# Optimization experiments

Hardware: AMD Instinct MI355X
Metric: run time of the kernel (lower is better)

The kernel has to match this reference:

```python
import jax, jax.numpy as jnp
import numpy as np

D_MODEL = 256; N_HEADS = 8; N_LEVELS = 4; N_POINTS = 4
D_HEAD = D_MODEL // N_HEADS


def setup_inputs() -> dict:
    key = jax.random.key(0)
    ks = jax.random.split(key, 8)
    N, Lq = 4, 4096
    shapes = np.array([4096, 2048, 1024, 512], dtype=np.int32)  # temporal lengths per level
    Len_in = int(shapes.sum())  # 7680
    start = np.concatenate([[0], np.cumsum(shapes)[:-1]]).astype(np.int32)
    HLP = N_HEADS * N_LEVELS * N_POINTS
    return {
        "query": jax.random.normal(ks[0], (N, Lq, D_MODEL), jnp.float32),
        "reference_points": jax.random.uniform(ks[1], (N, Lq, N_LEVELS, 1), jnp.float32),
        "input_flatten": jax.random.normal(ks[2], (N, Len_in, D_MODEL), jnp.float32),
        "input_spatial_shapes": jnp.asarray(shapes),
        "input_level_start_index": jnp.asarray(start),
        "W_off": jax.random.normal(ks[3], (D_MODEL, HLP), jnp.float32) * 0.01,
        "b_off": jax.random.normal(ks[4], (HLP,), jnp.float32) * 2.0,
        "W_aw": jax.random.normal(ks[5], (D_MODEL, HLP), jnp.float32) * 0.02,
        "b_aw": jnp.zeros((HLP,), jnp.float32),
        "W_v": jax.random.normal(ks[6], (D_MODEL, D_MODEL), jnp.float32) / np.sqrt(D_MODEL).astype(np.float32),
        "b_v": jnp.zeros((D_MODEL,), jnp.float32),
        "W_out": jax.random.normal(ks[7], (D_MODEL, D_MODEL), jnp.float32) / np.sqrt(D_MODEL).astype(np.float32),
        "b_out": jnp.zeros((D_MODEL,), jnp.float32),
    }


def reference(query, reference_points, input_flatten, input_spatial_shapes,
              input_level_start_index, W_off, b_off, W_aw, b_aw, W_v, b_v,
              W_out, b_out):
    N, Lq, C = query.shape
    M, L, P, Dh = N_HEADS, N_LEVELS, N_POINTS, D_HEAD
    S = input_flatten.shape[1]

    value = (input_flatten @ W_v + b_v).reshape(N, S, M, Dh)
    off = (query @ W_off + b_off).reshape(N, Lq, M, L, P)
    aw = jax.nn.softmax((query @ W_aw + b_aw).reshape(N, Lq, M, L * P), axis=-1)
    aw = aw.reshape(N, Lq, M, L, P)

    # reference_points last dim == 1 branch: loc = ref + off / T_l, in [0,1]
    T = input_spatial_shapes.astype(jnp.float32)[None, None, None, :, None]  # [1,1,1,L,1]
    loc = reference_points[:, :, None, :, None, 0] + off / T  # [N,Lq,M,L,P]

    # grid_sample(align_corners=False, padding_mode='border') along W with H=1, y=0.5:
    # pixel coord x = loc*T - 0.5, clamped to [0, T-1], then linear interp.
    x = jnp.clip(loc * T - 0.5, 0.0, T - 1.0)
    x0 = jnp.floor(x)
    w1 = x - x0                                   # frac weight for right neighbor
    i0 = x0.astype(jnp.int32)
    i1 = jnp.minimum(i0 + 1, input_spatial_shapes[None, None, None, :, None] - 1)
    base = input_level_start_index[None, None, None, :, None]
    g0 = i0 + base                                # global flattened indices [N,Lq,M,L,P]
    g1 = i1 + base

    v = value.transpose(0, 2, 1, 3)               # [N,M,S,Dh]

    def gather(idx):
        idxt = idx.transpose(0, 2, 1, 3, 4).reshape(N, M, Lq * L * P, 1)
        return jnp.take_along_axis(v, idxt, axis=2).reshape(N, M, Lq, L, P, Dh)

    s0 = gather(g0)
    s1 = gather(g1)
    w1t = w1.transpose(0, 2, 1, 3, 4)[..., None]   # [N,M,Lq,L,P,1]
    samp = s0 * (1.0 - w1t) + s1 * w1t             # [N,M,Lq,L,P,Dh]

    awt = aw.transpose(0, 2, 1, 3, 4)[..., None]
    out = (samp * awt).sum(axis=(3, 4))            # [N,M,Lq,Dh]
    out = out.transpose(0, 2, 1, 3).reshape(N, Lq, M * Dh)
    return out @ W_out + b_out
```

## Files before the change

kernel.cpp:

```cpp
#include <hip/hip_runtime.h>
#include <hip/hip_bf16.h>
#include <cstddef>
#include <cstdint>

#define D_MODEL   256
#define N_HEADS   8
#define N_LEVELS  4
#define N_POINTS  4
#define D_HEAD    32
#define HLP       128
#define NBATCH    4
#define LQ        4096
#define S_LEN     7680
#define QB        8

typedef __attribute__((ext_vector_type(8))) short  short8;
typedef __attribute__((ext_vector_type(4))) float  f32x4;
typedef __attribute__((ext_vector_type(8))) unsigned short ushort8;

__device__ __forceinline__ unsigned short f2bf(float x) {
    __hip_bfloat16 h = __float2bfloat16(x);
    return *reinterpret_cast<unsigned short*>(&h);
}
__device__ __forceinline__ float bf2f(unsigned short u) {
    unsigned int v = ((unsigned int)u) << 16;
    return *reinterpret_cast<float*>(&v);
}

__device__ __forceinline__ void gload_lds16(const void* g, void* l) {
    __builtin_amdgcn_global_load_lds(
        (const __attribute__((address_space(1))) void*)g,
        (__attribute__((address_space(3))) void*)l,
        16, 0, 0);
}

__global__ __launch_bounds__(256) void prep_kernel(
    const float* __restrict__ W_v,  const float* __restrict__ W_off,
    const float* __restrict__ W_aw, const float* __restrict__ W_out,
    const float* __restrict__ b_off, const float* __restrict__ b_aw,
    unsigned short* __restrict__ Wv_t, unsigned short* __restrict__ Wcat_t,
    unsigned short* __restrict__ Wout_t, float* __restrict__ bcat)
{
    __shared__ float t[64][65];
    const int z   = blockIdx.z;
    const int k0  = blockIdx.y * 64;
    const int n0  = blockIdx.x * 64;
    const int tid = threadIdx.x;

    const float* src; int srcN; int cs; unsigned short* dst;
    if (z == 0)      { src = W_v;   srcN = 256; cs = n0;       dst = Wv_t;  }
    else if (z == 2) { src = W_out; srcN = 256; cs = n0;       dst = Wout_t;}
    else if (n0 < 128){ src = W_off; srcN = 128; cs = n0;      dst = Wcat_t;}
    else             { src = W_aw;  srcN = 128; cs = n0 - 128; dst = Wcat_t;}

    #pragma unroll
    for (int i = 0; i < 16; ++i) {
        int idx = tid + i * 256;
        int kk = idx >> 6, nn = idx & 63;
        t[kk][nn] = src[(size_t)(k0 + kk) * srcN + cs + nn];
    }
    __syncthreads();
    #pragma unroll
    for (int i = 0; i < 16; ++i) {
        int idx = tid + i * 256;
        int nn = idx >> 6, kk = idx & 63;
        dst[(size_t)(n0 + nn) * 256 + k0 + kk] = f2bf(t[kk][nn]);
    }
    if (z == 1 && blockIdx.x == 0 && blockIdx.y == 0) {
        bcat[tid] = (tid < 128) ? b_off[tid] : b_aw[tid - 128];
    }
}

__global__ __launch_bounds__(256) void gemm_vp_kernel(
    const float* __restrict__ inflat, const float* __restrict__ query,
    const unsigned short* __restrict__ Wv_t, const unsigned short* __restrict__ Wcat_t,
    const float* __restrict__ b_v, const float* __restrict__ bcat,
    unsigned short* __restrict__ value3, float* __restrict__ P)
{
    __shared__ alignas(16) unsigned short Abuf[2][4][64][8];
    __shared__ alignas(16) unsigned short Bbuf[2][8][64][8];

    const int job = blockIdx.x;
    const bool is_val = (job < 960);
    const int jj   = is_val ? job : (job - 960);
    const int row0 = (jj >> 1) * 64;
    const int col0 = (jj & 1) * 128;
    const float* A = is_val ? inflat : query;
    const unsigned short* Bt = is_val ? Wv_t : Wcat_t;
    const float* bias = is_val ? b_v : bcat;

    const int tid  = threadIdx.x;
    const int lane = tid & 63;
    const int w    = tid >> 6;
    const int lr   = lane & 15;
    const int lk   = (lane >> 4) * 8;

    const int ar = tid >> 2;
    const int ak = (tid & 3) * 8;
    const int afrag = ar >> 4;
    const int alane = ((ak >> 3) << 4) | (ar & 15);
    const float* Arow = A + (size_t)(row0 + ar) * 256 + ak;
    const unsigned short* Bcol = Bt + (size_t)(col0 + lr) * 256 + lk;

    f32x4 acc[8] = {};

    float4 pa0 = *(const float4*)(Arow);
    float4 pa1 = *(const float4*)(Arow + 4);
    #pragma unroll
    for (int c = 0; c < 2; ++c) {
        const int in = w * 2 + c;
        gload_lds16(Bcol + (size_t)in * 16 * 256, &Bbuf[0][in][0][0]);
    }

    for (int kt = 0; kt < 8; ++kt) {
        const int cur = kt & 1;
        short8 pk;
        pk[0] = (short)f2bf(pa0.x); pk[1] = (short)f2bf(pa0.y);
        pk[2] = (short)f2bf(pa0.z); pk[3] = (short)f2bf(pa0.w);
        pk[4] = (short)f2bf(pa1.x); pk[5] = (short)f2bf(pa1.y);
        pk[6] = (short)f2bf(pa1.z); pk[7] = (short)f2bf(pa1.w);
        *(short8*)&Abuf[cur][afrag][alane][0] = pk;
        __syncthreads();

        if (kt < 7) {
            const int k1 = (kt + 1) * 32;
            pa0 = *(const float4*)(Arow + k1);
            pa1 = *(const float4*)(Arow + k1 + 4);
            #pragma unroll
            for (int c = 0; c < 2; ++c) {
                const int in = w * 2 + c;
                gload_lds16(Bcol + (size_t)in * 16 * 256 + k1, &Bbuf[1 - cur][in][0][0]);
            }
        }

        const short8 af = *(const short8*)&Abuf[cur][w][lane][0];
        #pragma unroll
        for (int j = 0; j < 8; ++j) {
            const short8 bf = *(const short8*)&Bbuf[cur][j][lane][0];
            acc[j] = __builtin_amdgcn_mfma_f32_16x16x32_bf16(af, bf, acc[j], 0, 0, 0);
        }
    }

    const int prow = (lane >> 4) * 4;
    const int pcol = lane & 15;
    const int rbase = row0 + w * 16 + prow;
    if (is_val) {
        const int n  = row0 / S_LEN;
        const int s0 = row0 - n * S_LEN + w * 16 + prow;
        #pragma unroll
        for (int j = 0; j < 8; ++j) {
            const int col = col0 + j * 16 + pcol;
            const float bs = bias[col];
            const int m = col >> 5, d = col & 31;
            unsigned short* dst = value3 + ((size_t)(n * 8 + m) * S_LEN + s0) * 32 + d;
            #pragma unroll
            for (int r = 0; r < 4; ++r)
                dst[(size_t)r * 32] = f2bf(acc[j][r] + bs);
        }
    } else {
        #pragma unroll
        for (int j = 0; j < 8; ++j) {
            const int col = col0 + j * 16 + pcol;
            const float bs = bias[col];
            #pragma unroll
            for (int r = 0; r < 4; ++r)
                P[(size_t)(rbase + r) * 256 + col] = acc[j][r] + bs;
        }
    }
}

__global__ __launch_bounds__(256) void sample_kernel(
    const float* __restrict__ P, const float* __restrict__ refp,
    const int* __restrict__ shapes, const int* __restrict__ lstart,
    const unsigned short* __restrict__ value3,
    unsigned short* __restrict__ tout)
{
    __shared__ int   sG0[QB][130];
    __shared__ float sW [QB][130];
    __shared__ float sA [QB][130];
    __shared__ int   glim[4];

    const int b    = blockIdx.x;
    const int xcd  = b & 7;
    const int n    = xcd >> 1;
    const int half = xcd & 1;
    const int slot = b >> 3;
    const int q0   = (slot * 2 + half) * QB;
    const int nq0  = n * LQ + q0;
    const int tid  = threadIdx.x;

    if (tid < 4) glim[tid] = lstart[tid] + shapes[tid] - 1;

    #pragma unroll
    for (int it = 0; it < 4; ++it) {
        const int idx = tid + it * 256;
        const int q   = idx >> 7;
        const int j   = idx & 127;
        const int l   = (j >> 2) & 3;
        const int nq  = nq0 + q;
        const float off   = __builtin_nontemporal_load(P + (size_t)nq * 256 + j);
        const float logit = __builtin_nontemporal_load(P + (size_t)nq * 256 + 128 + j);
        const float ref   = __builtin_nontemporal_load(refp + (size_t)nq * N_LEVELS + l);
        const int   sh    = shapes[l];
        const float Tf    = (float)sh;
        float x = ref * Tf + off - 0.5f;
        x = fminf(fmaxf(x, 0.0f), Tf - 1.0f);
        const float x0 = floorf(x);
        sG0[q][j] = (int)x0 + lstart[l];
        sW [q][j] = x - x0;
        sA [q][j] = logit;
    }
    __syncthreads();

    const int q  = tid >> 5;
    const int r  = tid & 31;
    const int m  = r >> 2;
    const int ql = r & 3;
    const unsigned short* vb =
        value3 + (size_t)(n * 8 + m) * S_LEN * 32 + ql * 8;

    float e[16];
    float mx = -1e30f;
    #pragma unroll
    for (int i = 0; i < 16; ++i) { e[i] = sA[q][m * 16 + i]; mx = fmaxf(mx, e[i]); }
    float s = 0.f;
    #pragma unroll
    for (int i = 0; i < 16; ++i) { e[i] = __expf(e[i] - mx); s += e[i]; }
    const float rs = 1.0f / s;

    float acc[8] = {};
    #pragma unroll
    for (int i = 0; i < 16; ++i) {
        const int j = m * 16 + i;
        const float a  = e[i] * rs;
        const float ww = sW[q][j];
        const int g0 = sG0[q][j];
        const int g1 = min(g0 + 1, glim[i >> 2]);
        const ushort8 u0 = *(const ushort8*)(vb + (size_t)g0 * 32);
        const ushort8 u1 = *(const ushort8*)(vb + (size_t)g1 * 32);
        #pragma unroll
        for (int d = 0; d < 8; ++d) {
            const float v0 = bf2f(u0[d]);
            const float v1 = bf2f(u1[d]);
            acc[d] += a * (v0 + ww * (v1 - v0));
        }
    }
    ushort8 o;
    #pragma unroll
    for (int d = 0; d < 8; ++d) o[d] = f2bf(acc[d]);
    __builtin_nontemporal_store(o,
        (ushort8*)(tout + (size_t)(nq0 + q) * 256 + m * 32 + ql * 8));
}

__global__ __launch_bounds__(256) void gemm_out_kernel(
    const unsigned short* __restrict__ A,
    const unsigned short* __restrict__ Bt,
    const float* __restrict__ bias,
    float* __restrict__ Cout)
{
    __shared__ alignas(16) unsigned short Abuf[2][4][64][8];
    __shared__ alignas(16) unsigned short Bbuf[2][8][64][8];

    const int jj   = blockIdx.x;
    const int row0 = (jj >> 1) * 64;
    const int col0 = (jj & 1) * 128;

    const int tid  = threadIdx.x;
    const int lane = tid & 63;
    const int w    = tid >> 6;
    const int lr   = lane & 15;
    const int lk   = (lane >> 4) * 8;

    const unsigned short* Arow = A + (size_t)(row0 + w * 16 + lr) * 256 + lk;
    const unsigned short* Bcol = Bt + (size_t)(col0 + lr) * 256 + lk;

    f32x4 acc[8] = {};

    gload_lds16(Arow, &Abuf[0][w][0][0]);
    #pragma unroll
    for (int c = 0; c < 2; ++c) {
        const int in = w * 2 + c;
        gload_lds16(Bcol + (size_t)in * 16 * 256, &Bbuf[0][in][0][0]);
    }

    for (int kt = 0; kt < 8; ++kt) {
        const int cur = kt & 1;
        __syncthreads();

        if (kt < 7) {
            const int k1 = (kt + 1) * 32;
            gload_lds16(Arow + k1, &Abuf[1 - cur][w][0][0]);
            #pragma unroll
            for (int c = 0; c < 2; ++c) {
                const int in = w * 2 + c;
                gload_lds16(Bcol + (size_t)in * 16 * 256 + k1, &Bbuf[1 - cur][in][0][0]);
            }
        }

        const short8 af = *(const short8*)&Abuf[cur][w][lane][0];
        #pragma unroll
        for (int j = 0; j < 8; ++j) {
            const short8 bf = *(const short8*)&Bbuf[cur][j][lane][0];
            acc[j] = __builtin_amdgcn_mfma_f32_16x16x32_bf16(af, bf, acc[j], 0, 0, 0);
        }
    }

    const int prow = (lane >> 4) * 4;
    const int pcol = lane & 15;
    const int rbase = row0 + w * 16 + prow;
    #pragma unroll
    for (int j = 0; j < 8; ++j) {
        const int col = col0 + j * 16 + pcol;
        const float bs = bias[col];
        #pragma unroll
        for (int r = 0; r < 4; ++r)
            Cout[(size_t)(rbase + r) * 256 + col] = acc[j][r] + bs;
    }
}

extern "C" void kernel_launch(void* const* d_in, const int* in_sizes, int n_in,
                              void* d_out, int out_size, void* d_ws, size_t ws_size,
                              hipStream_t stream)
{
    const float* query  = (const float*)d_in[0];
    const float* refp   = (const float*)d_in[1];
    const float* inflat = (const float*)d_in[2];
    const int*   shapes = (const int*)d_in[3];
    const int*   lstart = (const int*)d_in[4];
    const float* W_off  = (const float*)d_in[5];
    const float* b_off  = (const float*)d_in[6];
    const float* W_aw   = (const float*)d_in[7];
    const float* b_aw   = (const float*)d_in[8];
    const float* W_v    = (const float*)d_in[9];
    const float* b_v    = (const float*)d_in[10];
    const float* W_out  = (const float*)d_in[11];
    const float* b_out  = (const float*)d_in[12];

    const int M_val = NBATCH * S_LEN;
    const int M_q   = NBATCH * LQ;

    char* p = (char*)d_ws;
    unsigned short* value3 = (unsigned short*)p; p += (size_t)M_val * D_MODEL * 2;
    float*          P      = (float*)p;          p += (size_t)M_q * 256 * 4;
    unsigned short* tbuf   = (unsigned short*)p; p += (size_t)M_q * D_MODEL * 2;
    unsigned short* Wv_t   = (unsigned short*)p; p += 256 * 256 * 2;
    unsigned short* Wcat_t = (unsigned short*)p; p += 256 * 256 * 2;
    unsigned short* Wout_t = (unsigned short*)p; p += 256 * 256 * 2;
    float*          bcat   = (float*)p;          p += 256 * 4;

    prep_kernel<<<dim3(4, 4, 3), 256, 0, stream>>>(
        W_v, W_off, W_aw, W_out, b_off, b_aw, Wv_t, Wcat_t, Wout_t, bcat);
    gemm_vp_kernel<<<1472, 256, 0, stream>>>(
        inflat, query, Wv_t, Wcat_t, b_v, bcat, value3, P);
    sample_kernel<<<2048, 256, 0, stream>>>(
        P, refp, shapes, lstart, value3, tbuf);
    gemm_out_kernel<<<512, 256, 0, stream>>>(
        tbuf, Wout_t, b_out, (float*)d_out);
}
```

Measured before the change: 160.9 us.

## Assign one head per sampling block over 64 queries for value locality

The sampling kernel now gives each block a single head and 64 consecutive queries, instead of all 8 heads for 8 queries. Blocks are spread so that the XCD parity selects the head. Gathers from one block then stay inside one head's value slice, which should improve L2 locality. The prologue loads offsets and logits as float4 and writes them to LDS as vectors. The risk is narrower per-row P reads (64 bytes per query per block) and a grid mapping that must still match the launch size.

After: 163.6 us. No clear change (+1.7%).

```diff
diff --git a/kernel.cpp b/kernel.cpp
--- a/kernel.cpp
+++ b/kernel.cpp
@@ -12,10 +12,10 @@
 #define NBATCH    4
 #define LQ        4096
 #define S_LEN     7680
-#define QB        8
 
 typedef __attribute__((ext_vector_type(8))) short  short8;
 typedef __attribute__((ext_vector_type(4))) float  f32x4;
+typedef __attribute__((ext_vector_type(4))) int    i32x4;
 typedef __attribute__((ext_vector_type(8))) unsigned short ushort8;
 
 __device__ __forceinline__ unsigned short f2bf(float x) {
@@ -175,54 +175,71 @@
     const unsigned short* __restrict__ value3,
     unsigned short* __restrict__ tout)
 {
-    __shared__ int   sG0[QB][130];
-    __shared__ float sW [QB][130];
-    __shared__ float sA [QB][130];
+    __shared__ int   sG0[64][20];
+    __shared__ float sW [64][20];
+    __shared__ float sA [64][20];
     __shared__ int   glim[4];
 
     const int b    = blockIdx.x;
     const int xcd  = b & 7;
     const int n    = xcd >> 1;
-    const int half = xcd & 1;
-    const int slot = b >> 3;
-    const int q0   = (slot * 2 + half) * QB;
+    const int mpar = xcd & 1;
+    const int jb   = b >> 3;
+    const int m    = ((jb & 3) << 1) | mpar;
+    const int q0   = (jb >> 2) * 64;
     const int nq0  = n * LQ + q0;
     const int tid  = threadIdx.x;
 
     if (tid < 4) glim[tid] = lstart[tid] + shapes[tid] - 1;
 
-    #pragma unroll
-    for (int it = 0; it < 4; ++it) {
-        const int idx = tid + it * 256;
-        const int q   = idx >> 7;
-        const int j   = idx & 127;
-        const int l   = (j >> 2) & 3;
-        const int nq  = nq0 + q;
-        const float off   = __builtin_nontemporal_load(P + (size_t)nq * 256 + j);
-        const float logit = __builtin_nontemporal_load(P + (size_t)nq * 256 + 128 + j);
-        const float ref   = __builtin_nontemporal_load(refp + (size_t)nq * N_LEVELS + l);
+    {
+        const int q  = tid >> 2;
+        const int l  = tid & 3;
+        const int i0 = l * 4;
+        const int nq = nq0 + q;
+        const f32x4 off   = __builtin_nontemporal_load(
+            (const f32x4*)(P + (size_t)nq * 256 + m * 16 + i0));
+        const f32x4 logit = __builtin_nontemporal_load(
+            (const f32x4*)(P + (size_t)nq * 256 + 128 + m * 16 + i0));
+        const float ref   = refp[(size_t)nq * N_LEVELS + l];
         const int   sh    = shapes[l];
+        const int   ls    = lstart[l];
         const float Tf    = (float)sh;
-        float x = ref * Tf + off - 0.5f;
-        x = fminf(fmaxf(x, 0.0f), Tf - 1.0f);
-        const float x0 = floorf(x);
-        sG0[q][j] = (int)x0 + lstart[l];
-        sW [q][j] = x - x0;
-        sA [q][j] = logit;
+        i32x4 g4; f32x4 w4;
+        #pragma unroll
+        for (int k = 0; k < 4; ++k) {
+            float x = ref * Tf + off[k] - 0.5f;
+            x = fminf(fmaxf(x, 0.0f), Tf - 1.0f);
+            const float x0 = floorf(x);
+            g4[k] = (int)x0 + ls;
+            w4[k] = x - x0;
+        }
+        *(i32x4*)&sG0[q][i0] = g4;
+        *(f32x4*)&sW [q][i0] = w4;
+        *(f32x4*)&sA [q][i0] = logit;
     }
     __syncthreads();
 
-    const int q  = tid >> 5;
-    const int r  = tid & 31;
-    const int m  = r >> 2;
-    const int ql = r & 3;
+    const int q  = tid >> 2;
+    const int ql = tid & 3;
+    const int nq = nq0 + q;
     const unsigned short* vb =
         value3 + (size_t)(n * 8 + m) * S_LEN * 32 + ql * 8;
 
     float e[16];
+    {
+        const f32x4 a0 = *(const f32x4*)&sA[q][0];
+        const f32x4 a1 = *(const f32x4*)&sA[q][4];
+        const f32x4 a2 = *(const f32x4*)&sA[q][8];
+        const f32x4 a3 = *(const f32x4*)&sA[q][12];
+        #pragma unroll
+        for (int k = 0; k < 4; ++k) {
+            e[k] = a0[k]; e[4+k] = a1[k]; e[8+k] = a2[k]; e[12+k] = a3[k];
+        }
+    }
     float mx = -1e30f;
     #pragma unroll
-    for (int i = 0; i < 16; ++i) { e[i] = sA[q][m * 16 + i]; mx = fmaxf(mx, e[i]); }
+    for (int i = 0; i < 16; ++i) mx = fmaxf(mx, e[i]);
     float s = 0.f;
     #pragma unroll
     for (int i = 0; i < 16; ++i) { e[i] = __expf(e[i] - mx); s += e[i]; }
@@ -231,10 +248,9 @@
     float acc[8] = {};
     #pragma unroll
     for (int i = 0; i < 16; ++i) {
-        const int j = m * 16 + i;
         const float a  = e[i] * rs;
-        const float ww = sW[q][j];
-        const int g0 = sG0[q][j];
+        const float ww = sW[q][i];
+        const int g0 = sG0[q][i];
         const int g1 = min(g0 + 1, glim[i >> 2]);
         const ushort8 u0 = *(const ushort8*)(vb + (size_t)g0 * 32);
         const ushort8 u1 = *(const ushort8*)(vb + (size_t)g1 * 32);
@@ -249,7 +265,7 @@
     #pragma unroll
     for (int d = 0; d < 8; ++d) o[d] = f2bf(acc[d]);
     __builtin_nontemporal_store(o,
-        (ushort8*)(tout + (size_t)(nq0 + q) * 256 + m * 32 + ql * 8));
+        (ushort8*)(tout + (size_t)nq * 256 + m * 32 + ql * 8));
 }
 
 __global__ __launch_bounds__(256) void gemm_out_kernel(
```

## Fuse deformable sampling with output projection GEMM via LDS staging

Applied to the files above, without the earlier changes.

Merges the sampling kernel and the output-projection GEMM into one kernel. Each block now handles 16 queries, stages the sampled bf16 result in LDS and runs MFMA against W_out, read straight from global memory. This removes the intermediate tbuf round-trip through HBM and one kernel launch. The offset and logit loads are also vectorised to float4. In exchange, every block rereads the full W_out matrix (from cache), and the grid is halved to 1024 blocks, which lowers parallelism.

Measured after the change: 162.3 us. About the same (+0.9%).

```diff
diff --git a/kernel.cpp b/kernel.cpp
--- a/kernel.cpp
+++ b/kernel.cpp
@@ -12,10 +12,10 @@
 #define NBATCH    4
 #define LQ        4096
 #define S_LEN     7680
-#define QB        8
 
 typedef __attribute__((ext_vector_type(8))) short  short8;
 typedef __attribute__((ext_vector_type(4))) float  f32x4;
+typedef __attribute__((ext_vector_type(4))) int    i32x4;
 typedef __attribute__((ext_vector_type(8))) unsigned short ushort8;
 
 __device__ __forceinline__ unsigned short f2bf(float x) {
@@ -169,15 +169,18 @@
     }
 }
 
-__global__ __launch_bounds__(256) void sample_kernel(
+__global__ __launch_bounds__(256) void sample_out_kernel(
     const float* __restrict__ P, const float* __restrict__ refp,
     const int* __restrict__ shapes, const int* __restrict__ lstart,
     const unsigned short* __restrict__ value3,
-    unsigned short* __restrict__ tout)
+    const unsigned short* __restrict__ Wout_t,
+    const float* __restrict__ b_out,
+    float* __restrict__ Cout)
 {
-    __shared__ int   sG0[QB][130];
-    __shared__ float sW [QB][130];
-    __shared__ float sA [QB][130];
+    __shared__ int   sG0[16][132];
+    __shared__ float sW [16][132];
+    __shared__ float sA [16][132];
+    __shared__ alignas(16) unsigned short t_lds[16][264];
     __shared__ int   glim[4];
 
     const int b    = blockIdx.x;
@@ -185,136 +188,130 @@
     const int n    = xcd >> 1;
     const int half = xcd & 1;
     const int slot = b >> 3;
-    const int q0   = (slot * 2 + half) * QB;
+    const int q0   = (slot * 2 + half) * 16;
     const int nq0  = n * LQ + q0;
     const int tid  = threadIdx.x;
 
     if (tid < 4) glim[tid] = lstart[tid] + shapes[tid] - 1;
 
     #pragma unroll
-    for (int it = 0; it < 4; ++it) {
+    for (int it = 0; it < 2; ++it) {
         const int idx = tid + it * 256;
-        const int q   = idx >> 7;
-        const int j   = idx & 127;
-        const int l   = (j >> 2) & 3;
+        const int q   = idx >> 5;
+        const int sub = idx & 31;
+        const int m   = sub >> 2;
+        const int l   = sub & 3;
+        const int j0  = m * 16 + l * 4;
         const int nq  = nq0 + q;
-        const float off   = __builtin_nontemporal_load(P + (size_t)nq * 256 + j);
-        const float logit = __builtin_nontemporal_load(P + (size_t)nq * 256 + 128 + j);
-        const float ref   = __builtin_nontemporal_load(refp + (size_t)nq * N_LEVELS + l);
+        const f32x4 off   = __builtin_nontemporal_load(
+            (const f32x4*)(P + (size_t)nq * 256 + j0));
+        const f32x4 logit = __builtin_nontemporal_load(
+            (const f32x4*)(P + (size_t)nq * 256 + 128 + j0));
+        const float ref   = refp[(size_t)nq * N_LEVELS + l];
         const int   sh    = shapes[l];
+        const int   ls    = lstart[l];
         const float Tf    = (float)sh;
-        float x = ref * Tf + off - 0.5f;
-        x = fminf(fmaxf(x, 0.0f), Tf - 1.0f);
-        const float x0 = floorf(x);
-        sG0[q][j] = (int)x0 + lstart[l];
-        sW [q][j] = x - x0;
-        sA [q][j] = logit;
+        i32x4 g4; f32x4 w4;
+        #pragma unroll
+        for (int k = 0; k < 4; ++k) {
+            float x = ref * Tf + off[k] - 0.5f;
+            x = fminf(fmaxf(x, 0.0f), Tf - 1.0f);
+            const float x0 = floorf(x);
+            g4[k] = (int)x0 + ls;
+            w4[k] = x - x0;
+        }
+        *(i32x4*)&sG0[q][j0] = g4;
+        *(f32x4*)&sW [q][j0] = w4;
+        *(f32x4*)&sA [q][j0] = logit;
     }
     __syncthreads();
 
-    const int q  = tid >> 5;
-    const int r  = tid & 31;
-    const int m  = r >> 2;
-    const int ql = r & 3;
-    const unsigned short* vb =
-        value3 + (size_t)(n * 8 + m) * S_LEN * 32 + ql * 8;
-
-    float e[16];
-    float mx = -1e30f;
-    #pragma unroll
-    for (int i = 0; i < 16; ++i) { e[i] = sA[q][m * 16 + i]; mx = fmaxf(mx, e[i]); }
-    float s = 0.f;
-    #pragma unroll
-    for (int i = 0; i < 16; ++i) { e[i] = __expf(e[i] - mx); s += e[i]; }
-    const float rs = 1.0f / s;
-
-    float acc[8] = {};
-    #pragma unroll
-    for (int i = 0; i < 16; ++i) {
-        const int j = m * 16 + i;
-        const float a  = e[i] * rs;
-        const float ww = sW[q][j];
-        const int g0 = sG0[q][j];
-        const int g1 = min(g0 + 1, glim[i >> 2]);
-        const ushort8 u0 = *(const ushort8*)(vb + (size_t)g0 * 32);
-        const ushort8 u1 = *(const ushort8*)(vb + (size_t)g1 * 32);
-        #pragma unroll
-        for (int d = 0; d < 8; ++d) {
-            const float v0 = bf2f(u0[d]);
-            const float v1 = bf2f(u1[d]);
-            acc[d] += a * (v0 + ww * (v1 - v0));
-        }
-    }
-    ushort8 o;
-    #pragma unroll
-    for (int d = 0; d < 8; ++d) o[d] = f2bf(acc[d]);
-    __builtin_nontemporal_store(o,
-        (ushort8*)(tout + (size_t)(nq0 + q) * 256 + m * 32 + ql * 8));
-}
-
-__global__ __launch_bounds__(256) void gemm_out_kernel(
-    const unsigned short* __restrict__ A,
-    const unsigned short* __restrict__ Bt,
-    const float* __restrict__ bias,
-    float* __restrict__ Cout)
-{
-    __shared__ alignas(16) unsigned short Abuf[2][4][64][8];
-    __shared__ alignas(16) unsigned short Bbuf[2][8][64][8];
-
-    const int jj   = blockIdx.x;
-    const int row0 = (jj >> 1) * 64;
-    const int col0 = (jj & 1) * 128;
-
-    const int tid  = threadIdx.x;
+    #pragma unroll
+    for (int it = 0; it < 2; ++it) {
+        const int idx = tid + it * 256;
+        const int q   = idx >> 5;
+        const int sub = idx & 31;
+        const int m   = sub >> 2;
+        const int ql  = sub & 3;
+        const unsigned short* vb =
+            value3 + (size_t)(n * 8 + m) * S_LEN * 32 + ql * 8;
+
+        float e[16];
+        {
+            const f32x4 a0 = *(const f32x4*)&sA[q][m * 16 + 0];
+            const f32x4 a1 = *(const f32x4*)&sA[q][m * 16 + 4];
+            const f32x4 a2 = *(const f32x4*)&sA[q][m * 16 + 8];
+            const f32x4 a3 = *(const f32x4*)&sA[q][m * 16 + 12];
+            #pragma unroll
+            for (int k = 0; k < 4; ++k) {
+                e[k] = a0[k]; e[4+k] = a1[k]; e[8+k] = a2[k]; e[12+k] = a3[k];
+            }
+        }
+        float mx = -1e30f;
+        #pragma unroll
+        for (int i = 0; i < 16; ++i) mx = fmaxf(mx, e[i]);
+        float s = 0.f;
+        #pragma unroll
+        for (int i = 0; i < 16; ++i) { e[i] = __expf(e[i] - mx); s += e[i]; }
+        const float rs = 1.0f / s;
+
+        float acc[8] = {};
+        #pragma unroll
+        for (int i = 0; i < 16; ++i) {
+            const int j = m * 16 + i;
+            const float a  = e[i] * rs;
+            const float ww = sW[q][j];
+            const int g0 = sG0[q][j];
+            const int g1 = min(g0 + 1, glim[i >> 2]);
+            const ushort8 u0 = *(const ushort8*)(vb + (size_t)g0 * 32);
+            const ushort8 u1 = *(const ushort8*)(vb + (size_t)g1 * 32);
+            #pragma unroll
+            for (int d = 0; d < 8; ++d) {
+                const float v0 = bf2f(u0[d]);
+                const float v1 = bf2f(u1[d]);
+                acc[d] += a * (v0 + ww * (v1 - v0));
+            }
+        }
+        ushort8 o;
+        #pragma unroll
+        for (int d = 0; d < 8; ++d) o[d] = f2bf(acc[d]);
+        *(ushort8*)&t_lds[q][m * 32 + ql * 8] = o;
+    }
+    __syncthreads();
+
     const int lane = tid & 63;
-    const int w    = tid >> 6;
-    const int lr   = lane & 15;
-    const int lk   = (lane >> 4) * 8;
-
-    const unsigned short* Arow = A + (size_t)(row0 + w * 16 + lr) * 256 + lk;
-    const unsigned short* Bcol = Bt + (size_t)(col0 + lr) * 256 + lk;
-
-    f32x4 acc[8] = {};
-
-    gload_lds16(Arow, &Abuf[0][w][0][0]);
-    #pragma unroll
-    for (int c = 0; c < 2; ++c) {
-        const int in = w * 2 + c;
-        gload_lds16(Bcol + (size_t)in * 16 * 256, &Bbuf[0][in][0][0]);
-    }
-
-    for (int kt = 0; kt < 8; ++kt) {
-        const int cur = kt & 1;
-        __syncthreads();
-
-        if (kt < 7) {
-            const int k1 = (kt + 1) * 32;
-            gload_lds16(Arow + k1, &Abuf[1 - cur][w][0][0]);
-            #pragma unroll
-            for (int c = 0; c < 2; ++c) {
-                const int in = w * 2 + c;
-                gload_lds16(Bcol + (size_t)in * 16 * 256 + k1, &Bbuf[1 - cur][in][0][0]);
-            }
-        }
-
-        const short8 af = *(const short8*)&Abuf[cur][w][lane][0];
-        #pragma unroll
-        for (int j = 0; j < 8; ++j) {
-            const short8 bf = *(const short8*)&Bbuf[cur][j][lane][0];
-            acc[j] = __builtin_amdgcn_mfma_f32_16x16x32_bf16(af, bf, acc[j], 0, 0, 0);
+    const int wv   = tid >> 6;
+    const int arow = lane & 15;
+    const int kgrp = (lane >> 4) * 8;
+    const int n0   = wv * 64;
+
+    short8 af[8];
+    #pragma unroll
+    for (int kt = 0; kt < 8; ++kt)
+        af[kt] = *(const short8*)&t_lds[arow][kt * 32 + kgrp];
+
+    f32x4 oacc[4] = {};
+    #pragma unroll
+    for (int j = 0; j < 4; ++j) {
+        const unsigned short* bp =
+            Wout_t + (size_t)(n0 + j * 16 + arow) * 256 + kgrp;
+        #pragma unroll
+        for (int kt = 0; kt < 8; ++kt) {
+            const short8 bf = *(const short8*)(bp + kt * 32);
+            oacc[j] = __builtin_amdgcn_mfma_f32_16x16x32_bf16(af[kt], bf, oacc[j], 0, 0, 0);
         }
     }
 
     const int prow = (lane >> 4) * 4;
     const int pcol = lane & 15;
-    const int rbase = row0 + w * 16 + prow;
-    #pragma unroll
-    for (int j = 0; j < 8; ++j) {
-        const int col = col0 + j * 16 + pcol;
-        const float bs = bias[col];
+    #pragma unroll
+    for (int j = 0; j < 4; ++j) {
+        const int col = n0 + j * 16 + pcol;
+        const float bs = b_out[col];
         #pragma unroll
         for (int r = 0; r < 4; ++r)
-            Cout[(size_t)(rbase + r) * 256 + col] = acc[j][r] + bs;
+            __builtin_nontemporal_store(oacc[j][r] + bs,
+                Cout + (size_t)(nq0 + prow + r) * 256 + col);
     }
 }
 
@@ -342,7 +339,6 @@
     char* p = (char*)d_ws;
     unsigned short* value3 = (unsigned short*)p; p += (size_t)M_val * D_MODEL * 2;
     float*          P      = (float*)p;          p += (size_t)M_q * 256 * 4;
-    unsigned short* tbuf   = (unsigned short*)p; p += (size_t)M_q * D_MODEL * 2;
     unsigned short* Wv_t   = (unsigned short*)p; p += 256 * 256 * 2;
     unsigned short* Wcat_t = (unsigned short*)p; p += 256 * 256 * 2;
     unsigned short* Wout_t = (unsigned short*)p; p += 256 * 256 * 2;
@@ -352,8 +348,6 @@
         W_v, W_off, W_aw, W_out, b_off, b_aw, Wv_t, Wcat_t, Wout_t, bcat);
     gemm_vp_kernel<<<1472, 256, 0, stream>>>(
         inflat, query, Wv_t, Wcat_t, b_v, bcat, value3, P);
-    sample_kernel<<<2048, 256, 0, stream>>>(
-        P, refp, shapes, lstart, value3, tbuf);
-    gemm_out_kernel<<<512, 256, 0, stream>>>(
-        tbuf, Wout_t, b_out, (float*)d_out);
-}
+    sample_out_kernel<<<1024, 256, 0, stream>>>(
+        P, refp, shapes, lstart, value3, Wout_t, b_out, (float*)d_out);
+}
```
